# Optimization experiments

Measured on AMD Instinct MI355X. Metric: run time of the kernel, lower is better.

## Reference

```python
import jax, jax.numpy as jnp
import numpy as np

B, T, C, H = 2, 2048, 1024, 16
D = C // H
EPS = 1e-5

def _layer_norm(x, w, b):
    mu = jnp.mean(x, axis=-1, keepdims=True)
    var = jnp.var(x, axis=-1, keepdims=True)
    return (x - mu) * jax.lax.rsqrt(var + EPS) * w + b

def setup_inputs() -> dict:
    key = jax.random.key(0)
    ks = jax.random.split(key, 8)
    s = 0.02
    return {
        "x": jax.random.normal(ks[0], (B, T, C), jnp.float32),
        "ln1_w": jnp.ones((C,), jnp.float32),
        "ln1_b": jnp.zeros((C,), jnp.float32),
        "wq": jax.random.normal(ks[1], (C, C), jnp.float32) * s,
        "bq": jnp.zeros((C,), jnp.float32),
        "wk": jax.random.normal(ks[2], (C, C), jnp.float32) * s,
        "bk": jnp.zeros((C,), jnp.float32),
        "wv": jax.random.normal(ks[3], (C, C), jnp.float32) * s,
        "bv": jnp.zeros((C,), jnp.float32),
        "wo": jax.random.normal(ks[4], (C, C), jnp.float32) * s,
        "bo": jnp.zeros((C,), jnp.float32),
        "ln2_w": jnp.ones((C,), jnp.float32),
        "ln2_b": jnp.zeros((C,), jnp.float32),
        "w1": jax.random.normal(ks[5], (C, 4 * C), jnp.float32) * s,
        "b1": jnp.zeros((4 * C,), jnp.float32),
        "w2": jax.random.normal(ks[6], (4 * C, C), jnp.float32) * s,
        "b2": jnp.zeros((C,), jnp.float32),
    }

def reference(x, ln1_w, ln1_b, wq, bq, wk, bk, wv, bv, wo, bo,
              ln2_w, ln2_b, w1, b1, w2, b2):
    # --- attention branch ---
    h = _layer_norm(x, ln1_w, ln1_b)
    q = (h @ wq + bq).reshape(B, T, H, D).transpose(0, 2, 1, 3)  # [B,H,T,D]
    k = (h @ wk + bk).reshape(B, T, H, D).transpose(0, 2, 1, 3)
    v = (h @ wv + bv).reshape(B, T, H, D).transpose(0, 2, 1, 3)
    att = jnp.einsum("bhqd,bhkd->bhqk", q, k) * (1.0 / np.sqrt(D))
    causal = jnp.tril(jnp.ones((T, T), dtype=bool))
    att = jnp.where(causal[None, None], att, jnp.float32(-jnp.inf))
    att = jax.nn.softmax(att, axis=-1)
    y = jnp.einsum("bhqk,bhkd->bhqd", att, v)
    y = y.transpose(0, 2, 1, 3).reshape(B, T, C)
    y = y @ wo + bo
    x = x + y
    # --- MLP branch ---
    h = _layer_norm(x, ln2_w, ln2_b)
    h = jax.nn.gelu(h @ w1 + b1, approximate=False)
    h = h @ w2 + b2
    return x + h
```

## Files before the change

kernel.cpp:

```cpp
#include <hip/hip_runtime.h>
#include <hip/hip_bf16.h>
#include <math.h>

#define B_  2
#define T_  2048
#define C_  1024
#define H_  16
#define D_  64
#define BT_ (B_*T_)

typedef __hip_bfloat16 bf16;
typedef short bf16x8 __attribute__((ext_vector_type(8)));
typedef float floatx4 __attribute__((ext_vector_type(4)));

struct alignas(8) bf4 { bf16 v[4]; };

#define GLOAD_LDS16(g, l) __builtin_amdgcn_global_load_lds(            \
    (const __attribute__((address_space(1))) void*)(g),                \
    (__attribute__((address_space(3))) void*)(l), 16, 0, 0)

__global__ __launch_bounds__(256) void ln_bf16_kernel(const float* __restrict__ x,
    const float* __restrict__ w, const float* __restrict__ b,
    bf16* __restrict__ out)
{
    __shared__ float ps[4], ps2[4];
    __shared__ float sm, srs;
    const int row = blockIdx.x;
    const int tid = threadIdx.x;
    float4 v = ((const float4*)(x + (size_t)row * C_))[tid];
    float s  = v.x + v.y + v.z + v.w;
    float s2 = v.x*v.x + v.y*v.y + v.z*v.z + v.w*v.w;
    for (int off = 32; off > 0; off >>= 1) {
        s  += __shfl_down(s,  off);
        s2 += __shfl_down(s2, off);
    }
    const int wid = tid >> 6;
    if ((tid & 63) == 0) { ps[wid] = s; ps2[wid] = s2; }
    __syncthreads();
    if (tid == 0) {
        float ts  = ps[0] + ps[1] + ps[2] + ps[3];
        float ts2 = ps2[0] + ps2[1] + ps2[2] + ps2[3];
        float mean = ts * (1.0f / C_);
        float var  = ts2 * (1.0f / C_) - mean * mean;
        sm  = mean;
        srs = rsqrtf(var + 1e-5f);
    }
    __syncthreads();
    const float mean = sm, rs = srs;
    float4 wv = ((const float4*)w)[tid];
    float4 bv = ((const float4*)b)[tid];
    bf4 o;
    o.v[0] = __float2bfloat16((v.x - mean) * rs * wv.x + bv.x);
    o.v[1] = __float2bfloat16((v.y - mean) * rs * wv.y + bv.y);
    o.v[2] = __float2bfloat16((v.z - mean) * rs * wv.z + bv.z);
    o.v[3] = __float2bfloat16((v.w - mean) * rs * wv.w + bv.w);
    *(bf4*)(out + (size_t)row * C_ + tid * 4) = o;
}

__device__ __forceinline__ void wconv_body(const float* __restrict__ W,
    bf16* __restrict__ Wt, int K, int N, int k0, int n0)
{
    __shared__ float L[64][65];
    const int t = threadIdx.x;
    const int r = t >> 4, c4 = t & 15;
    #pragma unroll
    for (int p = 0; p < 4; ++p) {
        const int kr = p * 16 + r;
        const float4 v = *(const float4*)(W + (size_t)(k0 + kr) * N + n0 + c4 * 4);
        L[kr][c4*4+0] = v.x; L[kr][c4*4+1] = v.y;
        L[kr][c4*4+2] = v.z; L[kr][c4*4+3] = v.w;
    }
    __syncthreads();
    #pragma unroll
    for (int p = 0; p < 4; ++p) {
        const int nr = p * 16 + r;
        bf4 o;
        o.v[0] = __float2bfloat16(L[c4*4+0][nr]);
        o.v[1] = __float2bfloat16(L[c4*4+1][nr]);
        o.v[2] = __float2bfloat16(L[c4*4+2][nr]);
        o.v[3] = __float2bfloat16(L[c4*4+3][nr]);
        *(bf4*)(Wt + (size_t)(n0 + nr) * K + k0 + c4 * 4) = o;
    }
}

__global__ __launch_bounds__(256) void wconv4_kernel(
    const float* __restrict__ wq, const float* __restrict__ wk,
    const float* __restrict__ wv, const float* __restrict__ wo,
    bf16* __restrict__ wqkvT, bf16* __restrict__ woT)
{
    const int z = blockIdx.z;
    const float* W = (z == 0) ? wq : (z == 1) ? wk : (z == 2) ? wv : wo;
    bf16* Wt = (z == 3) ? woT : wqkvT + (size_t)z * 1024 * 1024;
    wconv_body(W, Wt, 1024, 1024, blockIdx.x * 64, blockIdx.y * 64);
}

__global__ __launch_bounds__(256) void wconv2_kernel(
    const float* __restrict__ w1, const float* __restrict__ w2,
    bf16* __restrict__ w1T, bf16* __restrict__ w2T)
{
    if (blockIdx.z == 0)
        wconv_body(w1, w1T, 1024, 4096, blockIdx.x * 64, blockIdx.y * 64);
    else
        wconv_body(w2, w2T, 4096, 1024, blockIdx.y * 64, blockIdx.x * 64);
}

__global__ void bcat_kernel(const float* __restrict__ bq, const float* __restrict__ bk,
                            const float* __restrict__ bv, float* __restrict__ o)
{
    const int i = blockIdx.x * 256 + threadIdx.x;
    float v = (i < 1024) ? bq[i] : (i < 2048 ? bk[i - 1024] : bv[i - 2048]);
    o[i] = v;
}

__global__ __launch_bounds__(256) void splitk_reduce_kernel(
    float* __restrict__ out, const float* __restrict__ p1,
    const float* __restrict__ bias, const float* __restrict__ res)
{
    const size_t i = (size_t)blockIdx.x * 256 + threadIdx.x;
    float4 o = ((const float4*)out)[i];
    const float4 p = ((const float4*)p1)[i];
    const float4 bb = ((const float4*)bias)[i & (C_ / 4 - 1)];
    const float4 xx = ((const float4*)res)[i];
    o.x += p.x + bb.x + xx.x;
    o.y += p.y + bb.y + xx.y;
    o.z += p.z + bb.z + xx.z;
    o.w += p.w + bb.w + xx.w;
    ((float4*)out)[i] = o;
}

template<int TM, int TN, int BK>
__global__ __launch_bounds__(256) void mfma_gemm_t(
    const bf16* __restrict__ A, const bf16* __restrict__ Wt,
    const float* __restrict__ bias, const float* __restrict__ res,
    void* __restrict__ outv, bf16* __restrict__ vT, float* __restrict__ psplit,
    int M, int N, int K, int ldk, int mode)
{
    constexpr int MI = TM / 32;
    constexpr int NJ = TN / 32;
    constexpr int CPR = BK / 8;
    constexpr int NSLOT = (TM + TN) * CPR / 256;
    __shared__ __align__(16) bf16 smem[(TM + TN) * BK];
    bf16* As = smem;
    bf16* Bs = smem + TM * BK;
    const int tid = threadIdx.x;
    const int w = tid >> 6, l = tid & 63;
    const int fm = l & 15, qd = l >> 4;
    const int m0 = blockIdx.x * TM, n0 = blockIdx.y * TN;
    const int bz = blockIdx.z;
    const int wr = (w >> 1) * (TM / 2), wc = (w & 1) * (TN / 2);

    const bf16* Ab = A  + (size_t)bz * K;
    const bf16* Wb = Wt + (size_t)bz * K;

    const bf16* gsrc[NSLOT];
    bf16* ldst[NSLOT];
    #pragma unroll
    for (int p = 0; p < NSLOT; ++p) {
        const int s = tid + p * 256;
        if (s < TM * CPR) {
            const int row = s / CPR, pos = s % CPR;
            const int ch = pos ^ (row & (CPR - 1));
            gsrc[p] = Ab + (size_t)(m0 + row) * ldk + ch * 8;
            ldst[p] = As + s * 8;
        } else {
            const int s2 = s - TM * CPR;
            const int row = s2 / CPR, pos = s2 % CPR;
            const int ch = pos ^ (row & (CPR - 1));
            gsrc[p] = Wb + (size_t)(n0 + row) * ldk + ch * 8;
            ldst[p] = Bs + s2 * 8;
        }
    }

    floatx4 acc[MI][NJ] = {};

    const int nk = K / BK;
    for (int kk = 0; kk < nk; ++kk) {
        const size_t ko = (size_t)kk * BK;
        __syncthreads();
        #pragma unroll
        for (int p = 0; p < NSLOT; ++p)
            GLOAD_LDS16(gsrc[p] + ko, ldst[p]);
        __syncthreads();
        #pragma unroll
        for (int ks = 0; ks < BK / 32; ++ks) {
            bf16x8 af[MI], bfr[NJ];
            #pragma unroll
            for (int i = 0; i < MI; ++i) {
                const int row = wr + i * 16 + fm;
                af[i] = *(const bf16x8*)(As + row * BK
                        + (((ks * 4 + qd) ^ (row & (CPR - 1))) * 8));
            }
            #pragma unroll
            for (int j = 0; j < NJ; ++j) {
                const int row = wc + j * 16 + fm;
                bfr[j] = *(const bf16x8*)(Bs + row * BK
                        + (((ks * 4 + qd) ^ (row & (CPR - 1))) * 8));
            }
            #pragma unroll
            for (int i = 0; i < MI; ++i)
                #pragma unroll
                for (int j = 0; j < NJ; ++j)
                    acc[i][j] = __builtin_amdgcn_mfma_f32_16x16x32_bf16(
                        af[i], bfr[j], acc[i][j], 0, 0, 0);
        }
    }

    const int col0 = n0 + wc;
    const int row0 = m0 + wr;
    const bool isv = (mode == 3) && (col0 >= 2048);
    const bool bounce = (mode == 0) || (mode == 1) || (mode == 3 && !isv);
    __syncthreads();

    if (bounce) {
        constexpr int RM = TM / 2, RN = TN / 2, CHN = RN / 8;
        bf16* eb = smem + w * (RM * RN);
        #pragma unroll
        for (int j = 0; j < NJ; ++j) {
            const int col = col0 + j * 16 + fm;
            const float bb = bias[col];
            const bool isq = (mode == 3) && (col0 + j * 16 < 1024);
            const int lc = j * 16 + fm;
            #pragma unroll
            for (int i = 0; i < MI; ++i) {
                floatx4 a = acc[i][j];
                #pragma unroll
                for (int r = 0; r < 4; ++r) {
                    float vv = a[r] + bb;
                    if (mode == 1) {
                        float zz = vv * (0.7978845608f + 0.0356774081f * vv * vv);
                        zz = fminf(zz, 15.0f);
                        const float e = __expf(2.0f * zz);
                        vv = vv * (e / (e + 1.0f));
                    }
                    if (isq) vv *= 0.125f;
                    const int lr = i * 16 + qd * 4 + r;
                    const int pch = ((lc >> 3) + 2 * qd) & (CHN - 1);
                    eb[lr * RN + pch * 8 + (lc & 7)] = __float2bfloat16(vv);
                }
            }
        }
        bf16* o = (bf16*)outv;
        #pragma unroll
        for (int c = 0; c < RM * RN / 512; ++c) {
            const int idx = c * 64 + l;
            const int row = idx / CHN;
            const int c8  = idx % CHN;
            const int pch = (c8 + 2 * ((row >> 2) & 3)) & (CHN - 1);
            const bf16x8 vv = *(const bf16x8*)(eb + row * RN + pch * 8);
            *(bf16x8*)(o + (size_t)(row0 + row) * N + col0 + c8 * 8) = vv;
        }
    } else {
        #pragma unroll
        for (int j = 0; j < NJ; ++j) {
            const int col = col0 + j * 16 + fm;
            const float bb = bias[col];
            #pragma unroll
            for (int i = 0; i < MI; ++i) {
                const int row = row0 + i * 16 + qd * 4;
                floatx4 a = acc[i][j];
                if (mode == 4) {
                    float* o = bz ? psplit : (float*)outv;
                    #pragma unroll
                    for (int r = 0; r < 4; ++r)
                        o[(size_t)(row + r) * N + col] = a[r];
                } else if (mode == 2) {
                    float* o = (float*)outv;
                    #pragma unroll
                    for (int r = 0; r < 4; ++r)
                        o[(size_t)(row + r) * N + col] =
                            a[r] + bb + res[(size_t)(row + r) * N + col];
                } else {
                    bf4 pv;
                    #pragma unroll
                    for (int r = 0; r < 4; ++r) pv.v[r] = __float2bfloat16(a[r] + bb);
                    *(bf4*)(vT + (size_t)(col - 2048) * M + row) = pv;
                }
            }
        }
    }
}

__global__ __launch_bounds__(256) void attn_mfma_kernel(
    const bf16* __restrict__ qkv, const bf16* __restrict__ vT,
    bf16* __restrict__ y)
{
    const int pi = blockIdx.x, h = blockIdx.y, b = blockIdx.z;
    const int tid = threadIdx.x, w = tid >> 6, l = tid & 63;
    const int fm = l & 15, qd = l >> 4;
    const int qta = pi, qtb = 31 - pi;
    const float M0 = 3.0f;

    __shared__ __align__(16) bf16 Ks[4096];
    __shared__ __align__(16) bf16 Vs[4096];
    __shared__ __align__(16) bf16 Ps[8][1152];

    const int r0 = tid >> 2,         c0 = (tid & 3) ^ ((r0 >> 1) & 3);
    const int r1 = (tid + 256) >> 2, c1 = ((tid + 256) & 3) ^ ((r1 >> 1) & 3);
    const bf16* kbase = qkv + (size_t)(b * T_) * 3072 + 1024 + h * 64;
    const bf16* vbase = vT + (size_t)(h * 64) * BT_ + b * T_;
    const bf16* kg0 = kbase + (size_t)(r0 & 63) * 3072 + (r0 >> 6) * 32 + c0 * 8;
    const bf16* kg1 = kbase + (size_t)(r1 & 63) * 3072 + (r1 >> 6) * 32 + c1 * 8;
    const bf16* vg0 = vbase + (size_t)(r0 & 63) * BT_ + (r0 >> 6) * 32 + c0 * 8;
    const bf16* vg1 = vbase + (size_t)(r1 & 63) * BT_ + (r1 >> 6) * 32 + c1 * 8;
    bf16* ksl0 = Ks + (size_t)(w * 64) * 8;
    bf16* ksl1 = Ks + (size_t)(w * 64 + 256) * 8;
    bf16* vsl0 = Vs + (size_t)(w * 64) * 8;
    bf16* vsl1 = Vs + (size_t)(w * 64 + 256) * 8;

    const bf16* qpa = qkv + (size_t)(b * T_ + qta * 64 + w * 16 + fm) * 3072 + h * 64 + qd * 8;
    const bf16* qpb = qkv + (size_t)(b * T_ + qtb * 64 + w * 16 + fm) * 3072 + h * 64 + qd * 8;
    const bf16x8 qa0 = *(const bf16x8*)qpa, qa1 = *(const bf16x8*)(qpa + 32);
    const bf16x8 qb0 = *(const bf16x8*)qpb, qb1 = *(const bf16x8*)(qpb + 32);

    const int qba = qta * 64 + w * 16 + qd * 4;
    const int qbb = qtb * 64 + w * 16 + qd * 4;
    const int sw = (qd ^ ((fm >> 1) & 3)) * 8;

    float la[4] = {}, lb[4] = {};
    floatx4 Oa[4] = {}, Ob[4] = {};
    bf16* psa = &Ps[w * 2][0];
    bf16* psb = &Ps[w * 2 + 1][0];

    auto tile = [&](const bf16x8 q0, const bf16x8 q1, float* lsum,
                    floatx4* O, bf16* ps, const int kt, const int qt, const int qb) {
        floatx4 S[4];
        #pragma unroll
        for (int nt = 0; nt < 4; ++nt) {
            const int rr = nt * 16 + fm;
            const bf16x8 k0 = *(const bf16x8*)(Ks + rr * 32 + sw);
            const bf16x8 k1 = *(const bf16x8*)(Ks + (64 + rr) * 32 + sw);
            floatx4 s = {};
            s = __builtin_amdgcn_mfma_f32_16x16x32_bf16(q0, k0, s, 0, 0, 0);
            s = __builtin_amdgcn_mfma_f32_16x16x32_bf16(q1, k1, s, 0, 0, 0);
            S[nt] = s;
        }
        if (kt == qt) {
            #pragma unroll
            for (int nt = 0; nt < 4; ++nt) {
                const int key = kt * 64 + nt * 16 + fm;
                #pragma unroll
                for (int r = 0; r < 4; ++r)
                    if (key > qb + r) S[nt][r] = -1e30f;
            }
        }
        #pragma unroll
        for (int nt = 0; nt < 4; ++nt)
            #pragma unroll
            for (int r = 0; r < 4; ++r) {
                const float p = __expf(S[nt][r] - M0);
                lsum[r] += p;
                ps[(qd * 4 + r) * 72 + nt * 16 + fm] = __float2bfloat16(p);
            }
        #pragma unroll
        for (int s2 = 0; s2 < 2; ++s2) {
            const bf16x8 pf = *(const bf16x8*)(ps + fm * 72 + s2 * 32 + qd * 8);
            #pragma unroll
            for (int nt = 0; nt < 4; ++nt) {
                const bf16x8 vf =
                    *(const bf16x8*)(Vs + (s2 * 64 + nt * 16 + fm) * 32 + sw);
                O[nt] = __builtin_amdgcn_mfma_f32_16x16x32_bf16(pf, vf, O[nt], 0, 0, 0);
            }
        }
    };

    for (int kt = 0; kt <= qtb; ++kt) {
        const size_t kOff = (size_t)kt * 64 * 3072;
        const size_t vOff = (size_t)kt * 64;
        __syncthreads();
        GLOAD_LDS16(kg0 + kOff, ksl0);
        GLOAD_LDS16(kg1 + kOff, ksl1);
        GLOAD_LDS16(vg0 + vOff, vsl0);
        GLOAD_LDS16(vg1 + vOff, vsl1);
        __syncthreads();
        tile(qb0, qb1, lb, Ob, psb, kt, qtb, qbb);
        if (kt <= qta)
            tile(qa0, qa1, la, Oa, psa, kt, qta, qba);
    }

    #pragma unroll
    for (int mk = 1; mk < 16; mk <<= 1)
        #pragma unroll
        for (int r = 0; r < 4; ++r) {
            la[r] += __shfl_xor(la[r], mk);
            lb[r] += __shfl_xor(lb[r], mk);
        }

    #pragma unroll
    for (int r = 0; r < 4; ++r) {
        const float inva = 1.0f / la[r];
        const float invb = 1.0f / lb[r];
        const size_t rowa = (size_t)(b * T_) + qba + r;
        const size_t rowb = (size_t)(b * T_) + qbb + r;
        #pragma unroll
        for (int nt = 0; nt < 4; ++nt) {
            y[rowa * C_ + h * 64 + nt * 16 + fm] = __float2bfloat16(Oa[nt][r] * inva);
            y[rowb * C_ + h * 64 + nt * 16 + fm] = __float2bfloat16(Ob[nt][r] * invb);
        }
    }
}

extern "C" void kernel_launch(void* const* d_in, const int* in_sizes, int n_in,
                              void* d_out, int out_size, void* d_ws, size_t ws_size,
                              hipStream_t stream)
{
    const float* x     = (const float*)d_in[0];
    const float* ln1_w = (const float*)d_in[1];
    const float* ln1_b = (const float*)d_in[2];
    const float* wq    = (const float*)d_in[3];
    const float* bq    = (const float*)d_in[4];
    const float* wk    = (const float*)d_in[5];
    const float* bk    = (const float*)d_in[6];
    const float* wv    = (const float*)d_in[7];
    const float* bv    = (const float*)d_in[8];
    const float* wo    = (const float*)d_in[9];
    const float* bo    = (const float*)d_in[10];
    const float* ln2_w = (const float*)d_in[11];
    const float* ln2_b = (const float*)d_in[12];
    const float* w1    = (const float*)d_in[13];
    const float* b1    = (const float*)d_in[14];
    const float* w2    = (const float*)d_in[15];
    const float* b2    = (const float*)d_in[16];
    float* out = (float*)d_out;

    char* ws = (char*)d_ws;
    const size_t MB = 1024 * 1024;
    bf16*  wqkvT = (bf16*)(ws);
    bf16*  woT   = (bf16*)(ws + 6 * MB);
    bf16*  w1T   = (bf16*)(ws + 8 * MB);
    bf16*  w2T   = (bf16*)(ws + 16 * MB);
    float* bqkv  = (float*)(ws + 24 * MB);
    bf16*  h     = (bf16*)(ws + 24 * MB + 65536);
    bf16*  qkv   = (bf16*)(ws + 32 * MB + 65536);
    bf16*  vT    = (bf16*)(ws + 56 * MB + 65536);
    bf16*  y     = (bf16*)(ws + 64 * MB + 65536);
    float* x2    = (float*)(ws + 72 * MB + 65536);
    bf16*  u     = qkv;
    float* p1    = (float*)ws;

    wconv4_kernel<<<dim3(16, 16, 4), 256, 0, stream>>>(wq, wk, wv, wo, wqkvT, woT);
    wconv2_kernel<<<dim3(16, 64, 2), 256, 0, stream>>>(w1, w2, w1T, w2T);
    bcat_kernel<<<12, 256, 0, stream>>>(bq, bk, bv, bqkv);

    ln_bf16_kernel<<<BT_, 256, 0, stream>>>(x, ln1_w, ln1_b, h);
    mfma_gemm_t<128, 128, 64><<<dim3(32, 24), 256, 0, stream>>>(
        h, wqkvT, bqkv, nullptr, qkv, vT, nullptr, BT_, 3072, C_, C_, 3);
    attn_mfma_kernel<<<dim3(16, H_, B_), 256, 0, stream>>>(qkv, vT, y);
    mfma_gemm_t<128, 64, 64><<<dim3(32, 16), 256, 0, stream>>>(
        y, woT, bo, x, x2, nullptr, nullptr, BT_, C_, C_, C_, 2);

    ln_bf16_kernel<<<BT_, 256, 0, stream>>>(x2, ln2_w, ln2_b, h);
    mfma_gemm_t<128, 128, 64><<<dim3(32, 32), 256, 0, stream>>>(
        h, w1T, b1, nullptr, u, nullptr, nullptr, BT_, 4 * C_, C_, C_, 1);
    mfma_gemm_t<128, 128, 64><<<dim3(32, 8, 2), 256, 0, stream>>>(
        u, w2T, b2, nullptr, out, nullptr, p1, BT_, C_, 2 * C_, 4 * C_, 4);
    splitk_reduce_kernel<<<BT_ * C_ / 1024, 256, 0, stream>>>(out, p1, b2, x2);
}
```

Before: 364.4 us.

## Add 256x256-tile 8-wave phased MFMA GEMM for QKV and FC1 projections

Introduces a new GEMM kernel with 256x256 output tiles, 512 threads and double-buffered LDS loaded through global_load_lds. Each K step is split into four MFMA phases that interleave the prefetch of the next tile, using explicit barriers, waitcnts and setprio. The epilogue stages results through LDS so global stores are coalesced 16-byte writes. The larger tiles aim to raise operand reuse and cut global and LDS traffic per flop, but they give far fewer workgroups (192 and 256) on a many-CU GPU, which risks underfilling the device.

```diff
diff --git a/kernel.cpp b/kernel.cpp
--- a/kernel.cpp
+++ b/kernel.cpp
@@ -280,6 +280,185 @@
     }
 }
 
+
+#define G8_BARRIER() do {                                   \
+    __builtin_amdgcn_sched_barrier(0);                      \
+    asm volatile("" ::: "memory");                          \
+    __builtin_amdgcn_s_barrier();                           \
+    asm volatile("" ::: "memory");                          \
+    __builtin_amdgcn_sched_barrier(0);                      \
+  } while (0)
+
+#define G8_WAIT_LGKM0() do {                                        \
+    asm volatile("s_waitcnt lgkmcnt(0)" ::: "memory");              \
+    __builtin_amdgcn_sched_barrier(0);                              \
+  } while (0)
+
+#define G8_WAIT_VM(n) asm volatile("s_waitcnt vmcnt(" #n ")" ::: "memory")
+
+#define G8_PHASE(Aq, Bq, G, VW)                                                \
+  do {                                                                         \
+    const bf16* pa0 = smem + cur * BUF + aof0 + (Aq) * 8192;                   \
+    const bf16* pa1 = smem + cur * BUF + aof1 + (Aq) * 8192;                   \
+    const bf16* pb0 = smem + cur * BUF + bof0 + (Bq) * 2048;                   \
+    const bf16* pb1 = smem + cur * BUF + bof1 + (Bq) * 2048;                   \
+    bf16x8 af[4][2], bv[2][2];                                                 \
+    _Pragma("unroll")                                                          \
+    for (int i = 0; i < 4; ++i) {                                              \
+      af[i][0] = *(const bf16x8*)(pa0 + i * 1024);                             \
+      af[i][1] = *(const bf16x8*)(pa1 + i * 1024);                             \
+    }                                                                          \
+    _Pragma("unroll")                                                          \
+    for (int jj = 0; jj < 2; ++jj) {                                           \
+      bv[jj][0] = *(const bf16x8*)(pb0 + jj * 1024);                           \
+      bv[jj][1] = *(const bf16x8*)(pb1 + jj * 1024);                           \
+    }                                                                          \
+    if (st) {                                                                  \
+      GLOAD_LDS16(gsrc[(G)*2]     + ko, smem + nb * BUF + lof[(G)*2]);         \
+      GLOAD_LDS16(gsrc[(G)*2 + 1] + ko, smem + nb * BUF + lof[(G)*2 + 1]);     \
+    }                                                                          \
+    G8_BARRIER();                                                              \
+    G8_WAIT_LGKM0();                                                           \
+    __builtin_amdgcn_s_setprio(1);                                             \
+    _Pragma("unroll")                                                          \
+    for (int i = 0; i < 4; ++i)                                                \
+      _Pragma("unroll")                                                        \
+      for (int jj = 0; jj < 2; ++jj) {                                         \
+        acc[(Aq)*4+i][(Bq)*2+jj] = __builtin_amdgcn_mfma_f32_16x16x32_bf16(    \
+            af[i][0], bv[jj][0], acc[(Aq)*4+i][(Bq)*2+jj], 0, 0, 0);           \
+        acc[(Aq)*4+i][(Bq)*2+jj] = __builtin_amdgcn_mfma_f32_16x16x32_bf16(    \
+            af[i][1], bv[jj][1], acc[(Aq)*4+i][(Bq)*2+jj], 0, 0, 0);           \
+      }                                                                        \
+    __builtin_amdgcn_s_setprio(0);                                             \
+    VW;                                                                        \
+    G8_BARRIER();                                                              \
+  } while (0)
+
+template<int MODE>
+__global__ __launch_bounds__(512, 2) void gemm8_t(
+    const bf16* __restrict__ A, const bf16* __restrict__ Wt,
+    const float* __restrict__ bias, bf16* __restrict__ out,
+    bf16* __restrict__ vT, int M, int N, int K)
+{
+    constexpr int BUF = 32768;
+    __shared__ __align__(16) bf16 smem[2 * BUF];
+
+    const int tid = threadIdx.x;
+    const int w = tid >> 6, l = tid & 63;
+    const int fm = l & 15, qd = l >> 4;
+    const int wm = w >> 2, wn = w & 3;
+
+    const int nbx = gridDim.x;
+    const int nwg = nbx * gridDim.y;
+    const int bid = blockIdx.y * nbx + blockIdx.x;
+    const int cpx = nwg >> 3;
+    const int swz = (bid & 7) * cpx + (bid >> 3);
+    const int m0 = (swz % nbx) * 256;
+    const int n0 = (swz / nbx) * 256;
+
+    const bf16* gsrc[8];
+    int lof[8];
+    #pragma unroll
+    for (int g = 0; g < 4; ++g) {
+        const bf16* gb = (g < 2) ? (Wt + (size_t)(n0 + (g & 1) * 128) * K)
+                                 : (A  + (size_t)(m0 + (g & 1) * 128) * K);
+        const int lbase = (g < 2) ? (16384 + (g & 1) * 8192) : ((g & 1) * 8192);
+        #pragma unroll
+        for (int s = 0; s < 2; ++s) {
+            const int c = tid + s * 512;
+            const int row = c >> 3, pos = c & 7;
+            const int ch = pos ^ (row & 7);
+            gsrc[g * 2 + s] = gb + (size_t)row * K + ch * 8;
+            lof[g * 2 + s] = lbase + c * 8;
+        }
+    }
+
+    const int sw0 = qd ^ (fm & 7);
+    const int aof0 = (wm * 64 + fm) * 64 + sw0 * 8;
+    const int aof1 = (wm * 64 + fm) * 64 + (sw0 ^ 4) * 8;
+    const int bof0 = 16384 + (wn * 64 + fm) * 64 + sw0 * 8;
+    const int bof1 = 16384 + (wn * 64 + fm) * 64 + (sw0 ^ 4) * 8;
+
+    floatx4 acc[8][4] = {};
+
+    #pragma unroll
+    for (int s = 0; s < 8; ++s)
+        GLOAD_LDS16(gsrc[s], smem + lof[s]);
+    G8_WAIT_VM(2);
+    G8_BARRIER();
+
+    const int nt = K / 64;
+    int cur = 0;
+    for (int t = 0; t < nt; ++t, cur ^= 1) {
+        const bool st = (t + 1 < nt);
+        const int nb = cur ^ 1;
+        const size_t ko = (size_t)(t + 1) * 64;
+        G8_PHASE(0, 0, 0, ;);
+        G8_PHASE(0, 1, 1, do { if (st) { G8_WAIT_VM(4); } else { G8_WAIT_VM(0); } } while (0));
+        G8_PHASE(1, 0, 2, ;);
+        G8_PHASE(1, 1, 3, G8_WAIT_VM(2));
+    }
+
+    G8_WAIT_VM(0);
+    G8_BARRIER();
+
+    const int colb = n0 + wn * 64;
+    if (MODE == 3 && colb >= 2048) {
+        #pragma unroll
+        for (int jf = 0; jf < 4; ++jf) {
+            const int col = colb + jf * 16 + fm;
+            const float bb = bias[col];
+            #pragma unroll
+            for (int f = 0; f < 8; ++f) {
+                const int row = m0 + (f >> 2) * 128 + wm * 64 + (f & 3) * 16 + qd * 4;
+                bf4 pv;
+                #pragma unroll
+                for (int r = 0; r < 4; ++r)
+                    pv.v[r] = __float2bfloat16(acc[f][jf][r] + bb);
+                *(bf4*)(vT + (size_t)(col - 2048) * M + row) = pv;
+            }
+        }
+    } else {
+        const float scale = (MODE == 3 && colb < 1024) ? 0.125f : 1.0f;
+        bf16* eb = smem + w * 8192;
+        #pragma unroll
+        for (int jf = 0; jf < 4; ++jf) {
+            const int col = colb + jf * 16 + fm;
+            const float bb = bias[col];
+            const int lc = jf * 16 + fm;
+            const int pch = ((lc >> 3) + 2 * qd) & 7;
+            #pragma unroll
+            for (int f = 0; f < 8; ++f) {
+                const int lr = (f & 3) * 16 + qd * 4;
+                #pragma unroll
+                for (int r = 0; r < 4; ++r) {
+                    float vv = acc[f][jf][r] + bb;
+                    if (MODE == 1) {
+                        float zz = vv * (0.7978845608f + 0.0356774081f * vv * vv);
+                        zz = fminf(zz, 15.0f);
+                        const float e = __expf(2.0f * zz);
+                        vv = vv * (e / (e + 1.0f));
+                    }
+                    vv *= scale;
+                    eb[(f >> 2) * 4096 + (lr + r) * 64 + pch * 8 + (lc & 7)] =
+                        __float2bfloat16(vv);
+                }
+            }
+        }
+        #pragma unroll
+        for (int p = 0; p < 2; ++p)
+            #pragma unroll
+            for (int c = 0; c < 8; ++c) {
+                const int idx = c * 64 + l;
+                const int row = idx >> 3, c8 = idx & 7;
+                const int pch = (c8 + 2 * ((row >> 2) & 3)) & 7;
+                const bf16x8 vv = *(const bf16x8*)(eb + p * 4096 + row * 64 + pch * 8);
+                const int rowg = m0 + p * 128 + wm * 64 + row;
+                *(bf16x8*)(out + (size_t)rowg * N + colb + c8 * 8) = vv;
+            }
+    }
+}
+
 __global__ __launch_bounds__(256) void attn_mfma_kernel(
     const bf16* __restrict__ qkv, const bf16* __restrict__ vT,
     bf16* __restrict__ y)
@@ -442,15 +621,15 @@
     bcat_kernel<<<12, 256, 0, stream>>>(bq, bk, bv, bqkv);
 
     ln_bf16_kernel<<<BT_, 256, 0, stream>>>(x, ln1_w, ln1_b, h);
-    mfma_gemm_t<128, 128, 64><<<dim3(32, 24), 256, 0, stream>>>(
-        h, wqkvT, bqkv, nullptr, qkv, vT, nullptr, BT_, 3072, C_, C_, 3);
+    gemm8_t<3><<<dim3(16, 12), 512, 0, stream>>>(
+        h, wqkvT, bqkv, qkv, vT, BT_, 3072, C_);
     attn_mfma_kernel<<<dim3(16, H_, B_), 256, 0, stream>>>(qkv, vT, y);
     mfma_gemm_t<128, 64, 64><<<dim3(32, 16), 256, 0, stream>>>(
         y, woT, bo, x, x2, nullptr, nullptr, BT_, C_, C_, C_, 2);
 
     ln_bf16_kernel<<<BT_, 256, 0, stream>>>(x2, ln2_w, ln2_b, h);
-    mfma_gemm_t<128, 128, 64><<<dim3(32, 32), 256, 0, stream>>>(
-        h, w1T, b1, nullptr, u, nullptr, nullptr, BT_, 4 * C_, C_, C_, 1);
+    gemm8_t<1><<<dim3(16, 16), 512, 0, stream>>>(
+        h, w1T, b1, u, nullptr, BT_, 4 * C_, C_);
     mfma_gemm_t<128, 128, 64><<<dim3(32, 8, 2), 256, 0, stream>>>(
         u, w2T, b2, nullptr, out, nullptr, p1, BT_, C_, 2 * C_, 4 * C_, 4);
     splitk_reduce_kernel<<<BT_ * C_ / 1024, 256, 0, stream>>>(out, p1, b2, x2);
```

Measured after the change: 364.8 us. No clear change (+0.1%).
